# Optimization experiments

Hardware: AMD Instinct MI355X
Metric: run time of the kernel (lower is better)

Reference implementation:

```python
import jax, jax.numpy as jnp
import numpy as np

N = 8192      # atoms
B = 64        # molecules
E = 262144    # edges
S = 4         # species
NMAX = 8      # radial basis size
CUT = 5.0     # cutoff radius
AVG_ATOMS = 128.0
E_SCALE = 1.0
PS_DIM = (S * NMAX) ** 2 * 4  # l_max=3 -> 4 l channels -> 4096
H1, H2 = 1024, 1024
OUT = 1


def _sph_harm(u):
    # real spherical harmonics up to l=3, input unit vectors [E,3] -> [E,16]
    x, y, z = u[:, 0], u[:, 1], u[:, 2]
    x2, y2, z2 = x * x, y * y, z * z
    return jnp.stack([
        0.28209479 * jnp.ones_like(x),
        0.48860251 * y, 0.48860251 * z, 0.48860251 * x,
        1.09254843 * x * y, 1.09254843 * y * z, 0.31539157 * (3.0 * z2 - 1.0),
        1.09254843 * x * z, 0.54627422 * (x2 - y2),
        0.59004359 * y * (3.0 * x2 - y2), 2.89061144 * x * y * z,
        0.45704579 * y * (5.0 * z2 - 1.0), 0.37317633 * z * (5.0 * z2 - 3.0),
        0.45704579 * x * (5.0 * z2 - 1.0), 1.44530572 * z * (x2 - y2),
        0.59004359 * x * (x2 - 3.0 * y2),
    ], axis=-1)


def setup_inputs() -> dict:
    key = jax.random.key(0)
    ks = jax.random.split(key, 12)
    positions = jax.random.normal(ks[0], (N, 3), dtype=jnp.float32) * 1.5  # dense cloud so many pairs < CUT
    cells = jnp.tile(20.0 * jnp.eye(3, dtype=jnp.float32)[None], (B, 1, 1))
    numbers = jax.random.randint(ks[1], (N,), 0, S)
    edge_indices = jax.random.randint(ks[2], (2, E), 0, N)
    edge_offsets = jnp.zeros((E, 3), dtype=jnp.float32)
    batch = jnp.arange(N) // (N // B)
    gamma = 1.0 + 0.1 * jax.random.normal(ks[3], (PS_DIM,), dtype=jnp.float32)
    beta = 0.1 * jax.random.normal(ks[4], (PS_DIM,), dtype=jnp.float32)
    W_ps = jax.random.normal(ks[5], (PS_DIM, OUT), dtype=jnp.float32) / np.sqrt(PS_DIM)
    W1 = jax.random.normal(ks[6], (PS_DIM, H1), dtype=jnp.float32) / np.sqrt(PS_DIM)
    W2 = jax.random.normal(ks[7], (H1, H2), dtype=jnp.float32) / np.sqrt(H1)
    W3 = jax.random.normal(ks[8], (H2, OUT), dtype=jnp.float32) / np.sqrt(H2)
    W_comp = jax.random.normal(ks[9], (S, OUT), dtype=jnp.float32) / np.sqrt(S)
    return dict(positions=positions, cells=cells, numbers=numbers,
                edge_indices=edge_indices, edge_offsets=edge_offsets, batch=batch,
                gamma=gamma, beta=beta, W_ps=W_ps, W1=W1, W2=W2, W3=W3, W_comp=W_comp)


def reference(positions, cells, numbers, edge_indices, edge_offsets, batch,
              gamma, beta, W_ps, W1, W2, W3, W_comp):
    i, j = edge_indices[0], edge_indices[1]  # center, neighbor
    # periodic shift: fractional offsets through the cell of the center's molecule
    shift = jnp.einsum('ec,ecd->ed', edge_offsets, cells[batch[i]])
    rvec = positions[j] - positions[i] + shift                      # [E,3]
    r = jnp.sqrt(jnp.sum(rvec * rvec, axis=-1) + 1e-12)             # [E]
    u = rvec / r[:, None]
    fc = 0.5 * (jnp.cos(jnp.pi * jnp.minimum(r, CUT) / CUT) + 1.0) * (r < CUT)
    n = jnp.arange(1, NMAX + 1, dtype=positions.dtype)
    R = fc[:, None] * jnp.sin(jnp.pi * n[None, :] * r[:, None] / CUT) / r[:, None]  # [E,NMAX]
    Y = _sph_harm(u)                                                # [E,16]
    edge_feat = R[:, :, None] * Y[:, None, :]                       # [E,NMAX,16]
    # spherical expansion c[i, species(j), n, lm] via scatter-add
    seg = i * S + numbers[j]
    c = jax.ops.segment_sum(edge_feat, seg, num_segments=N * S)     # [N*S,NMAX,16]
    c = c.reshape(N, S * NMAX, 16)
    # power spectrum: contract over m within each l block
    bounds = [(0, 1), (1, 4), (4, 9), (9, 16)]
    p = [jnp.einsum('ixm,iym->ixy', c[:, :, s:e], c[:, :, s:e]) for s, e in bounds]
    ps = jnp.stack(p, axis=-1).reshape(N, PS_DIM)                   # [N,4096]
    # LayerNorm (eps=1e-5, affine)
    mu = jnp.mean(ps, axis=-1, keepdims=True)
    var = jnp.var(ps, axis=-1, keepdims=True)
    psn = (ps - mu) / jnp.sqrt(var + 1e-5) * gamma + beta
    # linear branch + MLP branch
    psl = psn @ W_ps                                                # [N,1]
    h = jax.nn.silu(psn @ W1)
    h = jax.nn.silu(h @ W2)
    psnn = h @ W3                                                   # [N,1]
    # pool atomic energies into per-molecule totals (index_add)
    energies = jax.ops.segment_sum(psl + psnn, batch, num_segments=B) / AVG_ATOMS
    # eval path: composition baseline
    comp = jax.ops.segment_sum(jax.nn.one_hot(numbers, S, dtype=psn.dtype), batch, num_segments=B)
    return energies * E_SCALE + comp @ W_comp                       # [B,1]
```

## Files before the change

kernel.cpp:

```cpp
#include <hip/hip_runtime.h>
#include <hip/hip_bf16.h>
#include <math.h>

#define N_ATOMS 8192
#define B_BATCH 64
#define E_EDGES 262144
#define S_SPEC 4
#define NMAX 8
#define PS_DIM 4096
#define PS_K 2304
#define H1_DIM 1024
#define CAP4 48
#define CUTR 5.0f
#define PI_F 3.14159265358979f

typedef __bf16 bf16;
typedef unsigned long long u64;
typedef float floatx4 __attribute__((ext_vector_type(4)));
typedef int intx8 __attribute__((ext_vector_type(8)));
typedef unsigned char u8;

__device__ __forceinline__ void g2lds16(const void* g, void* l) {
    __builtin_amdgcn_global_load_lds(
        (const __attribute__((address_space(1))) void*)g,
        (__attribute__((address_space(3))) void*)l, 16, 0, 0);
}

__device__ __forceinline__ int pk_fp8x4(float a, float b, float c, float d) {
    int lo = __builtin_amdgcn_cvt_pk_fp8_f32(a, b, 0, false);
    return __builtin_amdgcn_cvt_pk_fp8_f32(c, d, lo, true);
}

__global__ __launch_bounds__(256) void prep_kernel(
    const float* __restrict__ pos, const float* __restrict__ cells,
    const int* __restrict__ numbers, const int* __restrict__ ei,
    const float* __restrict__ eo, const int* __restrict__ batch,
    int* __restrict__ cnt, float4* __restrict__ bucket,
    const float* __restrict__ W1, const float* __restrict__ gamma,
    const float* __restrict__ beta, const float* __restrict__ Wps,
    const float* __restrict__ W2,
    u8* __restrict__ Wt1, u8* __restrict__ Wt2, float* __restrict__ b1,
    float* __restrict__ gw, float* __restrict__ S23, float* __restrict__ out)
{
    if (blockIdx.x < 1024) {
        if (blockIdx.x == 0 && threadIdx.x < B_BATCH) out[threadIdx.x] = 0.0f;
        int e = blockIdx.x * 256 + threadIdx.x;
        int i = ei[e];
        int j = ei[E_EDGES + e];
        int b = batch[i];
        const float* cell = cells + b * 9;
        float o0 = eo[e * 3 + 0], o1 = eo[e * 3 + 1], o2 = eo[e * 3 + 2];
        float rv[3];
        #pragma unroll
        for (int d = 0; d < 3; ++d) {
            float shift = o0 * cell[0 * 3 + d] + o1 * cell[1 * 3 + d] + o2 * cell[2 * 3 + d];
            rv[d] = pos[j * 3 + d] - pos[i * 3 + d] + shift;
        }
        float r2 = rv[0] * rv[0] + rv[1] * rv[1] + rv[2] * rv[2] + 1e-12f;
        if (r2 >= CUTR * CUTR) return;
        float r = sqrtf(r2);
        float a1 = r * (PI_F / CUTR);
        int sp = numbers[j];
        int q = i * S_SPEC + sp;
        int slot = atomicAdd(&cnt[q], 1);
        if (slot < CAP4)
            bucket[q * CAP4 + slot] = make_float4(rv[0], rv[1], rv[2], a1);
        return;
    }

    if (blockIdx.x == 4352) {
        __shared__ float rs[8][2];
        int t = threadIdx.x, lane = t & 63, wv = t >> 6;
        float s2 = 0.0f, s3 = 0.0f;
        #pragma unroll
        for (int it = 0; it < 4; ++it) {
            int p4 = it * 256 + t;
            float4 g = *(const float4*)(gamma + p4 * 4);
            float4 bt = *(const float4*)(beta + p4 * 4);
            float4 w = *(const float4*)(Wps + p4 * 4);
            float4 gwv = make_float4(g.x * w.x, g.y * w.y, g.z * w.z, g.w * w.w);
            *(float4*)(gw + p4 * 4) = gwv;
            s2 += gwv.x + gwv.y + gwv.z + gwv.w;
            s3 += bt.x * w.x + bt.y * w.y + bt.z * w.z + bt.w * w.w;
        }
        #pragma unroll
        for (int o = 32; o > 0; o >>= 1) {
            s2 += __shfl_down(s2, o);
            s3 += __shfl_down(s3, o);
        }
        if (lane == 0) { rs[wv][0] = s2; rs[wv][1] = s3; }
        __syncthreads();
        if (t == 0) {
            S23[0] = rs[0][0] + rs[1][0] + rs[2][0] + rs[3][0];
            S23[1] = rs[0][1] + rs[1][1] + rs[2][1] + rs[3][1];
        }
        return;
    }

    __shared__ float tbuf[32][33];
    __shared__ float bred[8][32];
    int wid = blockIdx.x - 1024;
    int by = wid & 31;
    int bx = wid >> 5;
    int tx = threadIdx.x & 31, ty = threadIdx.x >> 5;
    int n0 = by * 32;

    if (bx < 72) {
        int k0 = bx * 32;
        float bacc = 0.0f;
        for (int r = 0; r < 32; r += 8) {
            int kk = ty + r;
            int kp = k0 + kk;
            int u = kp >> 2, lb = kp & 3;
            float val = 0.0f;
            if (u < 528) {
                int x = 0;
                while ((x + 1) * (64 - x) / 2 <= u) ++x;
                int y = x + (u - x * (65 - x) / 2);
                int p1 = x * 128 + y * 4 + lb;
                float w1v = W1[(size_t)p1 * H1_DIM + n0 + tx];
                val = gamma[p1] * w1v;
                bacc += beta[p1] * w1v;
                if (x < y) {
                    int p2 = y * 128 + x * 4 + lb;
                    float w2v = W1[(size_t)p2 * H1_DIM + n0 + tx];
                    val += gamma[p2] * w2v;
                    bacc += beta[p2] * w2v;
                }
            }
            tbuf[kk][tx] = val;
        }
        bred[ty][tx] = bacc;
        __syncthreads();
        if (ty == 0) {
            float s = 0.0f;
            #pragma unroll
            for (int i = 0; i < 8; ++i) s += bred[i][tx];
            atomicAdd(&b1[n0 + tx], s);
        }
        if (threadIdx.x < 64) {
            int nl = threadIdx.x >> 1, cc = threadIdx.x & 1;
            int n = n0 + nl;
            unsigned int w[4];
            #pragma unroll
            for (int g = 0; g < 4; ++g) {
                int kb = cc * 16 + g * 4;
                w[g] = (unsigned int)pk_fp8x4(
                    tbuf[kb + 0][nl] * 64.0f, tbuf[kb + 1][nl] * 64.0f,
                    tbuf[kb + 2][nl] * 64.0f, tbuf[kb + 3][nl] * 64.0f);
            }
            int gc = (k0 >> 4) + cc;
            int gcs = (gc & ~7) | ((gc & 7) ^ (n & 7));
            *(uint4*)(Wt1 + (size_t)n * PS_K + (size_t)gcs * 16) =
                make_uint4(w[0], w[1], w[2], w[3]);
        }
    } else {
        int k0 = (bx - 72) * 32;
        #pragma unroll
        for (int r = 0; r < 32; r += 8)
            tbuf[ty + r][tx] = W2[(size_t)(k0 + ty + r) * H1_DIM + n0 + tx];
        __syncthreads();
        if (threadIdx.x < 64) {
            int nl = threadIdx.x >> 1, cc = threadIdx.x & 1;
            int n = n0 + nl;
            unsigned int w[4];
            #pragma unroll
            for (int g = 0; g < 4; ++g) {
                int kb = cc * 16 + g * 4;
                w[g] = (unsigned int)pk_fp8x4(
                    tbuf[kb + 0][nl] * 32.0f, tbuf[kb + 1][nl] * 32.0f,
                    tbuf[kb + 2][nl] * 32.0f, tbuf[kb + 3][nl] * 32.0f);
            }
            int gc = (k0 >> 4) + cc;
            int gcs = (gc & ~7) | ((gc & 7) ^ (n & 7));
            *(uint4*)(Wt2 + (size_t)n * H1_DIM + (size_t)gcs * 16) =
                make_uint4(w[0], w[1], w[2], w[3]);
        }
    }
}

__global__ __launch_bounds__(256) void accum_ps_kernel(
    const float4* __restrict__ bucket, const int* __restrict__ cnt,
    const float* __restrict__ gw, const float* __restrict__ S23,
    u8* __restrict__ psn, float* __restrict__ psl)
{
    __shared__ __align__(16) float cl[4][32 * 20];
    __shared__ __align__(16) u8 ps_s8[PS_K];
    __shared__ float red[12];

    int t = threadIdx.x;
    int wv = t >> 6, lane = t & 63;
    int atom0 = blockIdx.x * 4;

    {
        int atom = atom0 + wv;
        int sp_l = lane >> 4;
        int nidx = (lane >> 1) & 7;
        float nf = (float)(nidx + 1);
        int par = lane & 1;

        int myCnt = cnt[atom * S_SPEC + sp_l];
        if (myCnt > CAP4) myCnt = CAP4;
        int m1 = max(myCnt, __shfl_xor(myCnt, 16));
        int mx = max(m1, __shfl_xor(m1, 32));

        const float4* q = bucket + (size_t)(atom * S_SPEC + sp_l) * CAP4;
        float acc[8] = {};
        #pragma unroll 2
        for (int e = 0; e < mx; ++e) {
            float4 d = q[e];
            bool valid = e < myCnt;
            float a1 = d.w;
            float inv_r = (PI_F / CUTR) * __frcp_rn(a1);
            float fc = 0.5f * __cosf(a1) + 0.5f;
            float rn = fc * inv_r * __sinf(nf * a1);
            rn = valid ? rn : 0.0f;

            float x = d.x * inv_r, y = d.y * inv_r, z = d.z * inv_r;
            float x2 = x * x, y2 = y * y, z2 = z * z;
            float Ys[8];
            if (par == 0) {
                Ys[0] = 0.28209479f;
                Ys[1] = 0.48860251f * y;
                Ys[2] = 0.48860251f * z;
                Ys[3] = 0.48860251f * x;
                Ys[4] = 1.09254843f * x * y;
                Ys[5] = 1.09254843f * y * z;
                Ys[6] = 0.31539157f * (3.0f * z2 - 1.0f);
                Ys[7] = 1.09254843f * x * z;
            } else {
                Ys[0] = 0.54627422f * (x2 - y2);
                Ys[1] = 0.59004359f * y * (3.0f * x2 - y2);
                Ys[2] = 2.89061144f * x * y * z;
                Ys[3] = 0.45704579f * y * (5.0f * z2 - 1.0f);
                Ys[4] = 0.37317633f * z * (5.0f * z2 - 3.0f);
                Ys[5] = 0.45704579f * x * (5.0f * z2 - 1.0f);
                Ys[6] = 1.44530572f * z * (x2 - y2);
                Ys[7] = 0.59004359f * x * (x2 - 3.0f * y2);
            }
            #pragma unroll
            for (int k = 0; k < 8; ++k) acc[k] += rn * Ys[k];
        }
        int X = sp_l * 8 + nidx;
        float* dst = &cl[wv][X * 20 + par * 8];
        *(float4*)(dst + 0) = make_float4(acc[0], acc[1], acc[2], acc[3]);
        *(float4*)(dst + 4) = make_float4(acc[4], acc[5], acc[6], acc[7]);
    }
    if (t < 48) ((int*)ps_s8)[528 + t] = 0;
    __syncthreads();

    float S2c = S23[0], S3c = S23[1];

    for (int a = 0; a < 4; ++a) {
        int atom = atom0 + a;
        const float* cl_x = cl[a];

        int y = t & 31;
        int xb = t >> 5;
        float4 cya = *(const float4*)&cl_x[y * 20 + 0];
        float4 cyb = *(const float4*)&cl_x[y * 20 + 4];
        float4 cyc = *(const float4*)&cl_x[y * 20 + 8];
        float4 cyd = *(const float4*)&cl_x[y * 20 + 12];

        float ps[4][4];
        float sum = 0.0f, sumsq = 0.0f, S1 = 0.0f;
        #pragma unroll
        for (int q = 0; q < 4; ++q) {
            int x = xb + 8 * q;
            float4 xa = *(const float4*)&cl_x[x * 20 + 0];
            float4 xbv = *(const float4*)&cl_x[x * 20 + 4];
            float4 xc = *(const float4*)&cl_x[x * 20 + 8];
            float4 xd = *(const float4*)&cl_x[x * 20 + 12];
            float s0 = xa.x * cya.x;
            float s1 = xa.y * cya.y + xa.z * cya.z + xa.w * cya.w;
            float s2 = xbv.x * cyb.x + xbv.y * cyb.y + xbv.z * cyb.z + xbv.w * cyb.w
                     + xc.x * cyc.x;
            float s3 = xc.y * cyc.y + xc.z * cyc.z + xc.w * cyc.w
                     + xd.x * cyd.x + xd.y * cyd.y + xd.z * cyd.z + xd.w * cyd.w;
            ps[q][0] = s0; ps[q][1] = s1; ps[q][2] = s2; ps[q][3] = s3;
            sum += s0 + s1 + s2 + s3;
            sumsq += s0 * s0 + s1 * s1 + s2 * s2 + s3 * s3;
            int p = t + 256 * q;
            float4 gwv = *(const float4*)(gw + p * 4);
            S1 += s0 * gwv.x + s1 * gwv.y + s2 * gwv.z + s3 * gwv.w;
        }
        #pragma unroll
        for (int o = 32; o > 0; o >>= 1) {
            sum += __shfl_down(sum, o);
            sumsq += __shfl_down(sumsq, o);
            S1 += __shfl_down(S1, o);
        }
        if ((t & 63) == 0) { red[wv] = sum; red[4 + wv] = sumsq; red[8 + wv] = S1; }
        __syncthreads();
        float tot = red[0] + red[1] + red[2] + red[3];
        float totsq = red[4] + red[5] + red[6] + red[7];
        float S1t = red[8] + red[9] + red[10] + red[11];
        float mu = tot * (1.0f / PS_DIM);
        float var = totsq * (1.0f / PS_DIM) - mu * mu;
        float inv = rsqrtf(var + 1e-5f);
        if (t == 0) psl[atom] = inv * (S1t - mu * S2c) + S3c;

        #pragma unroll
        for (int q = 0; q < 4; ++q) {
            int p = t + 256 * q;
            float z0 = (ps[q][0] - mu) * inv;
            float z1 = (ps[q][1] - mu) * inv;
            float z2 = (ps[q][2] - mu) * inv;
            float z3 = (ps[q][3] - mu) * inv;
            int x = p >> 5, yy = p & 31;
            if (x <= yy) {
                int u = x * (65 - x) / 2 + (yy - x);
                ((int*)ps_s8)[u] = pk_fp8x4(z0, z1, z2, z3);
            }
        }
        __syncthreads();
        u8* rowp = psn + (size_t)atom * PS_K;
        if (t < PS_K / 16) {
            int gcs = (t & ~7) | ((t & 7) ^ (atom & 7));
            *(uint4*)(rowp + (size_t)gcs * 16) = *(const uint4*)(ps_s8 + (size_t)t * 16);
        }
    }
}

__global__ __launch_bounds__(256) void gemm_f8_kernel(
    const u8* __restrict__ A, const u8* __restrict__ Bt,
    u8* __restrict__ H, const float* __restrict__ b1,
    int M, int Nc, int K, float invs)
{
    __shared__ __align__(16) char smem[65536];
    int tid = threadIdx.x;
    int bm = blockIdx.x, bn = blockIdx.y;
    int wave = tid >> 6, lane = tid & 63;
    int wm = (wave >> 1) * 64, wn = (wave & 1) * 64;
    int lm = lane & 15, quad = lane >> 4;

    floatx4 acc[4][4] = {};
    const int rowA0 = bm * 128, rowB0 = bn * 128;
    const size_t stride = (size_t)K;
    const char* Ab = (const char*)A + (size_t)rowA0 * stride;
    const char* Bb = (const char*)Bt + (size_t)rowB0 * stride;
    const int sA = 0x7F7F7F7F, sB = 0x7F7F7F7F;

    for (int k0 = 0; k0 < K; k0 += 256) {
        #pragma unroll
        for (int s = 0; s < 8; ++s) {
            int L = s * 256 + tid;
            int row = L >> 4, boff = (L & 15) * 16;
            int lbase = (s * 256 + wave * 64) * 16;
            g2lds16(Ab + (size_t)row * stride + k0 + boff, smem + lbase);
        }
        #pragma unroll
        for (int s = 0; s < 8; ++s) {
            int L = s * 256 + tid;
            int row = L >> 4, boff = (L & 15) * 16;
            int lbase = (s * 256 + wave * 64) * 16;
            g2lds16(Bb + (size_t)row * stride + k0 + boff, smem + 32768 + lbase);
        }
        __syncthreads();
        int key = lm & 7;
        int c0 = (2 * quad) ^ key, c1 = (2 * quad + 1) ^ key;
        #pragma unroll
        for (int h = 0; h < 2; ++h) {
            intx8 af[4], bfr[4];
            #pragma unroll
            for (int mi = 0; mi < 4; ++mi) {
                const char* base = smem + (wm + mi * 16 + lm) * 256 + h * 128;
                uint4 lo = *(const uint4*)(base + c0 * 16);
                uint4 hi = *(const uint4*)(base + c1 * 16);
                af[mi][0] = lo.x; af[mi][1] = lo.y; af[mi][2] = lo.z; af[mi][3] = lo.w;
                af[mi][4] = hi.x; af[mi][5] = hi.y; af[mi][6] = hi.z; af[mi][7] = hi.w;
            }
            #pragma unroll
            for (int ni = 0; ni < 4; ++ni) {
                const char* base = smem + 32768 + (wn + ni * 16 + lm) * 256 + h * 128;
                uint4 lo = *(const uint4*)(base + c0 * 16);
                uint4 hi = *(const uint4*)(base + c1 * 16);
                bfr[ni][0] = lo.x; bfr[ni][1] = lo.y; bfr[ni][2] = lo.z; bfr[ni][3] = lo.w;
                bfr[ni][4] = hi.x; bfr[ni][5] = hi.y; bfr[ni][6] = hi.z; bfr[ni][7] = hi.w;
            }
            #pragma unroll
            for (int mi = 0; mi < 4; ++mi)
                #pragma unroll
                for (int ni = 0; ni < 4; ++ni)
                    acc[mi][ni] = __builtin_amdgcn_mfma_scale_f32_16x16x128_f8f6f4(
                        af[mi], bfr[ni], acc[mi][ni], 0, 0, 0, sA, 0, sB);
        }
        __syncthreads();
    }

    u8* Cs8 = (u8*)smem;
    #pragma unroll
    for (int mi = 0; mi < 4; ++mi)
        #pragma unroll
        for (int ni = 0; ni < 4; ++ni) {
            float bv = b1[bn * 128 + wn + ni * 16 + lm];
            #pragma unroll
            for (int r = 0; r < 4; ++r) {
                int row = wm + mi * 16 + quad * 4 + r;
                int col = wn + ni * 16 + lm;
                float v = acc[mi][ni][r] * invs + bv;
                v = v / (1.0f + __expf(-v));
                int pk = __builtin_amdgcn_cvt_pk_fp8_f32(v, 0.0f, 0, false);
                Cs8[row * 128 + col] = (u8)(pk & 0xFF);
            }
        }
    __syncthreads();
    #pragma unroll
    for (int c2 = 0; c2 < 4; ++c2) {
        int L = c2 * 256 + tid;
        int row = L >> 3, cc = L & 7;
        int gcs = cc ^ (row & 7);
        *(uint4*)(H + (size_t)(rowA0 + row) * Nc + (size_t)(bn * 8 + gcs) * 16) =
            *(const uint4*)(Cs8 + (size_t)L * 16);
    }
}

__global__ __launch_bounds__(256) void gemm2_fused_kernel(
    const u8* __restrict__ A, const u8* __restrict__ Bt,
    const float* __restrict__ W3, const float* __restrict__ psl,
    const int* __restrict__ numbers, const float* __restrict__ Wcomp,
    float* __restrict__ out, int Nc, int K, float invs)
{
    __shared__ __align__(16) char smem[65536];
    int tid = threadIdx.x;
    int bm = blockIdx.x, bn = blockIdx.y;
    int wave = tid >> 6, lane = tid & 63;
    int wm = (wave >> 1) * 64, wn = (wave & 1) * 64;
    int lm = lane & 15, quad = lane >> 4;

    floatx4 acc[4][4] = {};
    const int rowA0 = bm * 128, rowB0 = bn * 128;
    const size_t stride = (size_t)K;
    const char* Ab = (const char*)A + (size_t)rowA0 * stride;
    const char* Bb = (const char*)Bt + (size_t)rowB0 * stride;
    const int sA = 0x7F7F7F7F, sB = 0x7F7F7F7F;

    for (int k0 = 0; k0 < K; k0 += 256) {
        #pragma unroll
        for (int s = 0; s < 8; ++s) {
            int L = s * 256 + tid;
            int row = L >> 4, boff = (L & 15) * 16;
            int lbase = (s * 256 + wave * 64) * 16;
            g2lds16(Ab + (size_t)row * stride + k0 + boff, smem + lbase);
        }
        #pragma unroll
        for (int s = 0; s < 8; ++s) {
            int L = s * 256 + tid;
            int row = L >> 4, boff = (L & 15) * 16;
            int lbase = (s * 256 + wave * 64) * 16;
            g2lds16(Bb + (size_t)row * stride + k0 + boff, smem + 32768 + lbase);
        }
        __syncthreads();
        int key = lm & 7;
        int c0 = (2 * quad) ^ key, c1 = (2 * quad + 1) ^ key;
        #pragma unroll
        for (int h = 0; h < 2; ++h) {
            intx8 af[4], bfr[4];
            #pragma unroll
            for (int mi = 0; mi < 4; ++mi) {
                const char* base = smem + (wm + mi * 16 + lm) * 256 + h * 128;
                uint4 lo = *(const uint4*)(base + c0 * 16);
                uint4 hi = *(const uint4*)(base + c1 * 16);
                af[mi][0] = lo.x; af[mi][1] = lo.y; af[mi][2] = lo.z; af[mi][3] = lo.w;
                af[mi][4] = hi.x; af[mi][5] = hi.y; af[mi][6] = hi.z; af[mi][7] = hi.w;
            }
            #pragma unroll
            for (int ni = 0; ni < 4; ++ni) {
                const char* base = smem + 32768 + (wn + ni * 16 + lm) * 256 + h * 128;
                uint4 lo = *(const uint4*)(base + c0 * 16);
                uint4 hi = *(const uint4*)(base + c1 * 16);
                bfr[ni][0] = lo.x; bfr[ni][1] = lo.y; bfr[ni][2] = lo.z; bfr[ni][3] = lo.w;
                bfr[ni][4] = hi.x; bfr[ni][5] = hi.y; bfr[ni][6] = hi.z; bfr[ni][7] = hi.w;
            }
            #pragma unroll
            for (int mi = 0; mi < 4; ++mi)
                #pragma unroll
                for (int ni = 0; ni < 4; ++ni)
                    acc[mi][ni] = __builtin_amdgcn_mfma_scale_f32_16x16x128_f8f6f4(
                        af[mi], bfr[ni], acc[mi][ni], 0, 0, 0, sA, 0, sB);
        }
        __syncthreads();
    }

    float lt = 0.0f;
    #pragma unroll
    for (int ni = 0; ni < 4; ++ni) {
        float w3v = W3[bn * 128 + wn + ni * 16 + lm];
        #pragma unroll
        for (int mi = 0; mi < 4; ++mi)
            #pragma unroll
            for (int r = 0; r < 4; ++r) {
                float v = acc[mi][ni][r] * invs;
                v = v / (1.0f + __expf(-v));
                lt += v * w3v;
            }
    }
    #pragma unroll
    for (int o = 32; o > 0; o >>= 1) lt += __shfl_down(lt, o);
    float* wsum = (float*)smem;
    int* c4 = ((int*)smem) + 8;
    float* shp = ((float*)smem) + 12;
    if (tid < S_SPEC) c4[tid] = 0;
    if (lane == 0) wsum[wave] = lt;
    __syncthreads();
    if (tid == 0)
        atomicAdd(&out[bm],
                  (wsum[0] + wsum[1] + wsum[2] + wsum[3]) * (1.0f / 128.0f));
    if (bn == 0) {
        if (tid < 128) {
            int a = bm * 128 + tid;
            float e = psl[a];
            atomicAdd(&c4[numbers[a]], 1);
            #pragma unroll
            for (int o = 32; o > 0; o >>= 1) e += __shfl_down(e, o);
            if ((tid & 63) == 0) shp[tid >> 6] = e;
        }
        __syncthreads();
        if (tid == 0) {
            float r = (shp[0] + shp[1]) * (1.0f / 128.0f);
            #pragma unroll
            for (int s = 0; s < S_SPEC; ++s) r += (float)c4[s] * Wcomp[s];
            atomicAdd(&out[bm], r);
        }
    }
}

extern "C" void kernel_launch(void* const* d_in, const int* in_sizes, int n_in,
                              void* d_out, int out_size, void* d_ws, size_t ws_size,
                              hipStream_t stream)
{
    const float* positions = (const float*)d_in[0];
    const float* cells     = (const float*)d_in[1];
    const int*   numbers   = (const int*)d_in[2];
    const int*   ei        = (const int*)d_in[3];
    const float* eo        = (const float*)d_in[4];
    const int*   batch     = (const int*)d_in[5];
    const float* gamma     = (const float*)d_in[6];
    const float* beta      = (const float*)d_in[7];
    const float* W_ps      = (const float*)d_in[8];
    const float* W1        = (const float*)d_in[9];
    const float* W2        = (const float*)d_in[10];
    const float* W3        = (const float*)d_in[11];
    const float* W_comp    = (const float*)d_in[12];
    float* out = (float*)d_out;

    char* ws = (char*)d_ws;
    float4* bucket = (float4*)ws;  ws += (size_t)N_ATOMS * S_SPEC * CAP4 * 16;
    u8*    psn  = (u8*)ws;     ws += (size_t)N_ATOMS * PS_K;
    u8*    h1   = (u8*)ws;     ws += (size_t)N_ATOMS * H1_DIM;
    u8*    Wt1  = (u8*)ws;     ws += (size_t)H1_DIM * PS_K;
    u8*    Wt2  = (u8*)ws;     ws += (size_t)H1_DIM * H1_DIM;
    float* psl  = (float*)ws;  ws += (size_t)N_ATOMS * 4;
    int*   cnt  = (int*)ws;    ws += (size_t)N_ATOMS * S_SPEC * 4;
    float* b1   = (float*)ws;  ws += (size_t)H1_DIM * 4;
    float* gw   = (float*)ws;  ws += (size_t)PS_DIM * 4;
    float* S23  = (float*)ws;  ws += 2 * 4;

    hipMemsetAsync(cnt, 0, (N_ATOMS * S_SPEC + H1_DIM) * sizeof(int), stream);

    prep_kernel<<<4353, 256, 0, stream>>>(
        positions, cells, numbers, ei, eo, batch, cnt, bucket,
        W1, gamma, beta, W_ps, W2, Wt1, Wt2, b1, gw, S23, out);

    accum_ps_kernel<<<N_ATOMS / 4, 256, 0, stream>>>(
        bucket, cnt, gw, S23, psn, psl);

    gemm_f8_kernel<<<dim3(N_ATOMS / 128, H1_DIM / 128), 256, 0, stream>>>(
        psn, Wt1, h1, b1, N_ATOMS, H1_DIM, PS_K, 1.0f / 64.0f);

    gemm2_fused_kernel<<<dim3(N_ATOMS / 128, H1_DIM / 128), 256, 0, stream>>>(
        h1, Wt2, W3, psl, numbers, W_comp, out, H1_DIM, H1_DIM, 1.0f / 32.0f);
}
```

Measured before the change: 183.9 us.

## Fuse all stages into one persistent cooperative kernel with grid syncs

```diff
diff --git a/kernel.cpp b/kernel.cpp
--- a/kernel.cpp
+++ b/kernel.cpp
@@ -1,6 +1,9 @@
 #include <hip/hip_runtime.h>
 #include <hip/hip_bf16.h>
+#include <hip/hip_cooperative_groups.h>
 #include <math.h>
+
+namespace cg = cooperative_groups;
 
 #define N_ATOMS 8192
 #define B_BATCH 64
@@ -14,8 +17,6 @@
 #define CUTR 5.0f
 #define PI_F 3.14159265358979f
 
-typedef __bf16 bf16;
-typedef unsigned long long u64;
 typedef float floatx4 __attribute__((ext_vector_type(4)));
 typedef int intx8 __attribute__((ext_vector_type(8)));
 typedef unsigned char u8;
@@ -31,7 +32,7 @@
     return __builtin_amdgcn_cvt_pk_fp8_f32(c, d, lo, true);
 }
 
-__global__ __launch_bounds__(256) void prep_kernel(
+__global__ __launch_bounds__(256, 2) void fused_all(
     const float* __restrict__ pos, const float* __restrict__ cells,
     const int* __restrict__ numbers, const int* __restrict__ ei,
     const float* __restrict__ eo, const int* __restrict__ batch,
@@ -40,488 +41,506 @@
     const float* __restrict__ beta, const float* __restrict__ Wps,
     const float* __restrict__ W2,
     u8* __restrict__ Wt1, u8* __restrict__ Wt2, float* __restrict__ b1,
-    float* __restrict__ gw, float* __restrict__ S23, float* __restrict__ out)
-{
-    if (blockIdx.x < 1024) {
-        if (blockIdx.x == 0 && threadIdx.x < B_BATCH) out[threadIdx.x] = 0.0f;
-        int e = blockIdx.x * 256 + threadIdx.x;
-        int i = ei[e];
-        int j = ei[E_EDGES + e];
-        int b = batch[i];
-        const float* cell = cells + b * 9;
-        float o0 = eo[e * 3 + 0], o1 = eo[e * 3 + 1], o2 = eo[e * 3 + 2];
-        float rv[3];
-        #pragma unroll
-        for (int d = 0; d < 3; ++d) {
-            float shift = o0 * cell[0 * 3 + d] + o1 * cell[1 * 3 + d] + o2 * cell[2 * 3 + d];
-            rv[d] = pos[j * 3 + d] - pos[i * 3 + d] + shift;
-        }
-        float r2 = rv[0] * rv[0] + rv[1] * rv[1] + rv[2] * rv[2] + 1e-12f;
-        if (r2 >= CUTR * CUTR) return;
-        float r = sqrtf(r2);
-        float a1 = r * (PI_F / CUTR);
-        int sp = numbers[j];
-        int q = i * S_SPEC + sp;
-        int slot = atomicAdd(&cnt[q], 1);
-        if (slot < CAP4)
-            bucket[q * CAP4 + slot] = make_float4(rv[0], rv[1], rv[2], a1);
-        return;
-    }
-
-    if (blockIdx.x == 4352) {
-        __shared__ float rs[8][2];
-        int t = threadIdx.x, lane = t & 63, wv = t >> 6;
-        float s2 = 0.0f, s3 = 0.0f;
-        #pragma unroll
-        for (int it = 0; it < 4; ++it) {
-            int p4 = it * 256 + t;
-            float4 g = *(const float4*)(gamma + p4 * 4);
-            float4 bt = *(const float4*)(beta + p4 * 4);
-            float4 w = *(const float4*)(Wps + p4 * 4);
-            float4 gwv = make_float4(g.x * w.x, g.y * w.y, g.z * w.z, g.w * w.w);
-            *(float4*)(gw + p4 * 4) = gwv;
-            s2 += gwv.x + gwv.y + gwv.z + gwv.w;
-            s3 += bt.x * w.x + bt.y * w.y + bt.z * w.z + bt.w * w.w;
-        }
-        #pragma unroll
-        for (int o = 32; o > 0; o >>= 1) {
-            s2 += __shfl_down(s2, o);
-            s3 += __shfl_down(s3, o);
-        }
-        if (lane == 0) { rs[wv][0] = s2; rs[wv][1] = s3; }
-        __syncthreads();
-        if (t == 0) {
-            S23[0] = rs[0][0] + rs[1][0] + rs[2][0] + rs[3][0];
-            S23[1] = rs[0][1] + rs[1][1] + rs[2][1] + rs[3][1];
-        }
-        return;
-    }
-
-    __shared__ float tbuf[32][33];
-    __shared__ float bred[8][32];
-    int wid = blockIdx.x - 1024;
-    int by = wid & 31;
-    int bx = wid >> 5;
-    int tx = threadIdx.x & 31, ty = threadIdx.x >> 5;
-    int n0 = by * 32;
-
-    if (bx < 72) {
-        int k0 = bx * 32;
-        float bacc = 0.0f;
-        for (int r = 0; r < 32; r += 8) {
-            int kk = ty + r;
-            int kp = k0 + kk;
-            int u = kp >> 2, lb = kp & 3;
-            float val = 0.0f;
-            if (u < 528) {
-                int x = 0;
-                while ((x + 1) * (64 - x) / 2 <= u) ++x;
-                int y = x + (u - x * (65 - x) / 2);
-                int p1 = x * 128 + y * 4 + lb;
-                float w1v = W1[(size_t)p1 * H1_DIM + n0 + tx];
-                val = gamma[p1] * w1v;
-                bacc += beta[p1] * w1v;
-                if (x < y) {
-                    int p2 = y * 128 + x * 4 + lb;
-                    float w2v = W1[(size_t)p2 * H1_DIM + n0 + tx];
-                    val += gamma[p2] * w2v;
-                    bacc += beta[p2] * w2v;
-                }
-            }
-            tbuf[kk][tx] = val;
-        }
-        bred[ty][tx] = bacc;
-        __syncthreads();
-        if (ty == 0) {
-            float s = 0.0f;
-            #pragma unroll
-            for (int i = 0; i < 8; ++i) s += bred[i][tx];
-            atomicAdd(&b1[n0 + tx], s);
-        }
-        if (threadIdx.x < 64) {
-            int nl = threadIdx.x >> 1, cc = threadIdx.x & 1;
-            int n = n0 + nl;
-            unsigned int w[4];
-            #pragma unroll
-            for (int g = 0; g < 4; ++g) {
-                int kb = cc * 16 + g * 4;
-                w[g] = (unsigned int)pk_fp8x4(
-                    tbuf[kb + 0][nl] * 64.0f, tbuf[kb + 1][nl] * 64.0f,
-                    tbuf[kb + 2][nl] * 64.0f, tbuf[kb + 3][nl] * 64.0f);
-            }
-            int gc = (k0 >> 4) + cc;
-            int gcs = (gc & ~7) | ((gc & 7) ^ (n & 7));
-            *(uint4*)(Wt1 + (size_t)n * PS_K + (size_t)gcs * 16) =
-                make_uint4(w[0], w[1], w[2], w[3]);
-        }
-    } else {
-        int k0 = (bx - 72) * 32;
-        #pragma unroll
-        for (int r = 0; r < 32; r += 8)
-            tbuf[ty + r][tx] = W2[(size_t)(k0 + ty + r) * H1_DIM + n0 + tx];
-        __syncthreads();
-        if (threadIdx.x < 64) {
-            int nl = threadIdx.x >> 1, cc = threadIdx.x & 1;
-            int n = n0 + nl;
-            unsigned int w[4];
-            #pragma unroll
-            for (int g = 0; g < 4; ++g) {
-                int kb = cc * 16 + g * 4;
-                w[g] = (unsigned int)pk_fp8x4(
-                    tbuf[kb + 0][nl] * 32.0f, tbuf[kb + 1][nl] * 32.0f,
-                    tbuf[kb + 2][nl] * 32.0f, tbuf[kb + 3][nl] * 32.0f);
-            }
-            int gc = (k0 >> 4) + cc;
-            int gcs = (gc & ~7) | ((gc & 7) ^ (n & 7));
-            *(uint4*)(Wt2 + (size_t)n * H1_DIM + (size_t)gcs * 16) =
-                make_uint4(w[0], w[1], w[2], w[3]);
-        }
-    }
-}
-
-__global__ __launch_bounds__(256) void accum_ps_kernel(
-    const float4* __restrict__ bucket, const int* __restrict__ cnt,
-    const float* __restrict__ gw, const float* __restrict__ S23,
-    u8* __restrict__ psn, float* __restrict__ psl)
-{
-    __shared__ __align__(16) float cl[4][32 * 20];
-    __shared__ __align__(16) u8 ps_s8[PS_K];
-    __shared__ float red[12];
-
-    int t = threadIdx.x;
-    int wv = t >> 6, lane = t & 63;
-    int atom0 = blockIdx.x * 4;
-
-    {
-        int atom = atom0 + wv;
-        int sp_l = lane >> 4;
-        int nidx = (lane >> 1) & 7;
-        float nf = (float)(nidx + 1);
-        int par = lane & 1;
-
-        int myCnt = cnt[atom * S_SPEC + sp_l];
-        if (myCnt > CAP4) myCnt = CAP4;
-        int m1 = max(myCnt, __shfl_xor(myCnt, 16));
-        int mx = max(m1, __shfl_xor(m1, 32));
-
-        const float4* q = bucket + (size_t)(atom * S_SPEC + sp_l) * CAP4;
-        float acc[8] = {};
-        #pragma unroll 2
-        for (int e = 0; e < mx; ++e) {
-            float4 d = q[e];
-            bool valid = e < myCnt;
-            float a1 = d.w;
-            float inv_r = (PI_F / CUTR) * __frcp_rn(a1);
-            float fc = 0.5f * __cosf(a1) + 0.5f;
-            float rn = fc * inv_r * __sinf(nf * a1);
-            rn = valid ? rn : 0.0f;
-
-            float x = d.x * inv_r, y = d.y * inv_r, z = d.z * inv_r;
-            float x2 = x * x, y2 = y * y, z2 = z * z;
-            float Ys[8];
-            if (par == 0) {
-                Ys[0] = 0.28209479f;
-                Ys[1] = 0.48860251f * y;
-                Ys[2] = 0.48860251f * z;
-                Ys[3] = 0.48860251f * x;
-                Ys[4] = 1.09254843f * x * y;
-                Ys[5] = 1.09254843f * y * z;
-                Ys[6] = 0.31539157f * (3.0f * z2 - 1.0f);
-                Ys[7] = 1.09254843f * x * z;
-            } else {
-                Ys[0] = 0.54627422f * (x2 - y2);
-                Ys[1] = 0.59004359f * y * (3.0f * x2 - y2);
-                Ys[2] = 2.89061144f * x * y * z;
-                Ys[3] = 0.45704579f * y * (5.0f * z2 - 1.0f);
-                Ys[4] = 0.37317633f * z * (5.0f * z2 - 3.0f);
-                Ys[5] = 0.45704579f * x * (5.0f * z2 - 1.0f);
-                Ys[6] = 1.44530572f * z * (x2 - y2);
-                Ys[7] = 0.59004359f * x * (x2 - 3.0f * y2);
-            }
-            #pragma unroll
-            for (int k = 0; k < 8; ++k) acc[k] += rn * Ys[k];
-        }
-        int X = sp_l * 8 + nidx;
-        float* dst = &cl[wv][X * 20 + par * 8];
-        *(float4*)(dst + 0) = make_float4(acc[0], acc[1], acc[2], acc[3]);
-        *(float4*)(dst + 4) = make_float4(acc[4], acc[5], acc[6], acc[7]);
-    }
-    if (t < 48) ((int*)ps_s8)[528 + t] = 0;
-    __syncthreads();
-
-    float S2c = S23[0], S3c = S23[1];
-
-    for (int a = 0; a < 4; ++a) {
-        int atom = atom0 + a;
-        const float* cl_x = cl[a];
-
-        int y = t & 31;
-        int xb = t >> 5;
-        float4 cya = *(const float4*)&cl_x[y * 20 + 0];
-        float4 cyb = *(const float4*)&cl_x[y * 20 + 4];
-        float4 cyc = *(const float4*)&cl_x[y * 20 + 8];
-        float4 cyd = *(const float4*)&cl_x[y * 20 + 12];
-
-        float ps[4][4];
-        float sum = 0.0f, sumsq = 0.0f, S1 = 0.0f;
-        #pragma unroll
-        for (int q = 0; q < 4; ++q) {
-            int x = xb + 8 * q;
-            float4 xa = *(const float4*)&cl_x[x * 20 + 0];
-            float4 xbv = *(const float4*)&cl_x[x * 20 + 4];
-            float4 xc = *(const float4*)&cl_x[x * 20 + 8];
-            float4 xd = *(const float4*)&cl_x[x * 20 + 12];
-            float s0 = xa.x * cya.x;
-            float s1 = xa.y * cya.y + xa.z * cya.z + xa.w * cya.w;
-            float s2 = xbv.x * cyb.x + xbv.y * cyb.y + xbv.z * cyb.z + xbv.w * cyb.w
-                     + xc.x * cyc.x;
-            float s3 = xc.y * cyc.y + xc.z * cyc.z + xc.w * cyc.w
-                     + xd.x * cyd.x + xd.y * cyd.y + xd.z * cyd.z + xd.w * cyd.w;
-            ps[q][0] = s0; ps[q][1] = s1; ps[q][2] = s2; ps[q][3] = s3;
-            sum += s0 + s1 + s2 + s3;
-            sumsq += s0 * s0 + s1 * s1 + s2 * s2 + s3 * s3;
-            int p = t + 256 * q;
-            float4 gwv = *(const float4*)(gw + p * 4);
-            S1 += s0 * gwv.x + s1 * gwv.y + s2 * gwv.z + s3 * gwv.w;
-        }
-        #pragma unroll
-        for (int o = 32; o > 0; o >>= 1) {
-            sum += __shfl_down(sum, o);
-            sumsq += __shfl_down(sumsq, o);
-            S1 += __shfl_down(S1, o);
-        }
-        if ((t & 63) == 0) { red[wv] = sum; red[4 + wv] = sumsq; red[8 + wv] = S1; }
-        __syncthreads();
-        float tot = red[0] + red[1] + red[2] + red[3];
-        float totsq = red[4] + red[5] + red[6] + red[7];
-        float S1t = red[8] + red[9] + red[10] + red[11];
-        float mu = tot * (1.0f / PS_DIM);
-        float var = totsq * (1.0f / PS_DIM) - mu * mu;
-        float inv = rsqrtf(var + 1e-5f);
-        if (t == 0) psl[atom] = inv * (S1t - mu * S2c) + S3c;
-
-        #pragma unroll
-        for (int q = 0; q < 4; ++q) {
-            int p = t + 256 * q;
-            float z0 = (ps[q][0] - mu) * inv;
-            float z1 = (ps[q][1] - mu) * inv;
-            float z2 = (ps[q][2] - mu) * inv;
-            float z3 = (ps[q][3] - mu) * inv;
-            int x = p >> 5, yy = p & 31;
-            if (x <= yy) {
-                int u = x * (65 - x) / 2 + (yy - x);
-                ((int*)ps_s8)[u] = pk_fp8x4(z0, z1, z2, z3);
-            }
-        }
-        __syncthreads();
-        u8* rowp = psn + (size_t)atom * PS_K;
-        if (t < PS_K / 16) {
-            int gcs = (t & ~7) | ((t & 7) ^ (atom & 7));
-            *(uint4*)(rowp + (size_t)gcs * 16) = *(const uint4*)(ps_s8 + (size_t)t * 16);
-        }
-    }
-}
-
-__global__ __launch_bounds__(256) void gemm_f8_kernel(
-    const u8* __restrict__ A, const u8* __restrict__ Bt,
-    u8* __restrict__ H, const float* __restrict__ b1,
-    int M, int Nc, int K, float invs)
+    float* __restrict__ gw, float* __restrict__ S23,
+    u8* __restrict__ psn, float* __restrict__ psl, u8* __restrict__ h1,
+    const float* __restrict__ W3, const float* __restrict__ Wcomp,
+    float* __restrict__ out)
 {
     __shared__ __align__(16) char smem[65536];
-    int tid = threadIdx.x;
-    int bm = blockIdx.x, bn = blockIdx.y;
-    int wave = tid >> 6, lane = tid & 63;
-    int wm = (wave >> 1) * 64, wn = (wave & 1) * 64;
-    int lm = lane & 15, quad = lane >> 4;
-
-    floatx4 acc[4][4] = {};
-    const int rowA0 = bm * 128, rowB0 = bn * 128;
-    const size_t stride = (size_t)K;
-    const char* Ab = (const char*)A + (size_t)rowA0 * stride;
-    const char* Bb = (const char*)Bt + (size_t)rowB0 * stride;
-    const int sA = 0x7F7F7F7F, sB = 0x7F7F7F7F;
-
-    for (int k0 = 0; k0 < K; k0 += 256) {
+    cg::grid_group grid = cg::this_grid();
+    const int nblk = gridDim.x;
+    const int tid = threadIdx.x;
+
+    {
+        int total = N_ATOMS * S_SPEC + H1_DIM;
+        for (int idx = blockIdx.x * 256 + tid; idx < total; idx += nblk * 256)
+            cnt[idx] = 0;
+        if (blockIdx.x == 0 && tid < B_BATCH) out[tid] = 0.0f;
+    }
+    __threadfence();
+    grid.sync();
+
+    {
+        float (*tbuf)[33] = (float(*)[33])smem;
+        float (*bred)[32] = (float(*)[32])(smem + 4224);
+        float (*rs)[2]    = (float(*)[2])(smem + 5248);
+
+        for (int vb = blockIdx.x; vb < 4353; vb += nblk) {
+            if (vb < 1024) {
+                int e = vb * 256 + tid;
+                int i = ei[e];
+                int j = ei[E_EDGES + e];
+                int b = batch[i];
+                const float* cell = cells + b * 9;
+                float o0 = eo[e * 3 + 0], o1 = eo[e * 3 + 1], o2 = eo[e * 3 + 2];
+                float rv[3];
+                #pragma unroll
+                for (int d = 0; d < 3; ++d) {
+                    float shift = o0 * cell[0 * 3 + d] + o1 * cell[1 * 3 + d]
+                                + o2 * cell[2 * 3 + d];
+                    rv[d] = pos[j * 3 + d] - pos[i * 3 + d] + shift;
+                }
+                float r2 = rv[0] * rv[0] + rv[1] * rv[1] + rv[2] * rv[2] + 1e-12f;
+                if (r2 < CUTR * CUTR) {
+                    float r = sqrtf(r2);
+                    float a1 = r * (PI_F / CUTR);
+                    int sp = numbers[j];
+                    int q = i * S_SPEC + sp;
+                    int slot = atomicAdd(&cnt[q], 1);
+                    if (slot < CAP4)
+                        bucket[q * CAP4 + slot] = make_float4(rv[0], rv[1], rv[2], a1);
+                }
+                continue;
+            }
+            if (vb == 4352) {
+                int lane = tid & 63, wv = tid >> 6;
+                float s2 = 0.0f, s3 = 0.0f;
+                #pragma unroll
+                for (int it = 0; it < 4; ++it) {
+                    int p4 = it * 256 + tid;
+                    float4 g = *(const float4*)(gamma + p4 * 4);
+                    float4 bt = *(const float4*)(beta + p4 * 4);
+                    float4 w = *(const float4*)(Wps + p4 * 4);
+                    float4 gwv = make_float4(g.x * w.x, g.y * w.y, g.z * w.z, g.w * w.w);
+                    *(float4*)(gw + p4 * 4) = gwv;
+                    s2 += gwv.x + gwv.y + gwv.z + gwv.w;
+                    s3 += bt.x * w.x + bt.y * w.y + bt.z * w.z + bt.w * w.w;
+                }
+                #pragma unroll
+                for (int o = 32; o > 0; o >>= 1) {
+                    s2 += __shfl_down(s2, o);
+                    s3 += __shfl_down(s3, o);
+                }
+                if (lane == 0) { rs[wv][0] = s2; rs[wv][1] = s3; }
+                __syncthreads();
+                if (tid == 0) {
+                    S23[0] = rs[0][0] + rs[1][0] + rs[2][0] + rs[3][0];
+                    S23[1] = rs[0][1] + rs[1][1] + rs[2][1] + rs[3][1];
+                }
+                __syncthreads();
+                continue;
+            }
+            int wid = vb - 1024;
+            int by = wid & 31;
+            int bx = wid >> 5;
+            int tx = tid & 31, ty = tid >> 5;
+            int n0 = by * 32;
+
+            if (bx < 72) {
+                int k0 = bx * 32;
+                float bacc = 0.0f;
+                for (int r = 0; r < 32; r += 8) {
+                    int kk = ty + r;
+                    int kp = k0 + kk;
+                    int u = kp >> 2, lb = kp & 3;
+                    float val = 0.0f;
+                    if (u < 528) {
+                        int x = 0;
+                        while ((x + 1) * (64 - x) / 2 <= u) ++x;
+                        int y = x + (u - x * (65 - x) / 2);
+                        int p1 = x * 128 + y * 4 + lb;
+                        float w1v = W1[(size_t)p1 * H1_DIM + n0 + tx];
+                        val = gamma[p1] * w1v;
+                        bacc += beta[p1] * w1v;
+                        if (x < y) {
+                            int p2 = y * 128 + x * 4 + lb;
+                            float w2v = W1[(size_t)p2 * H1_DIM + n0 + tx];
+                            val += gamma[p2] * w2v;
+                            bacc += beta[p2] * w2v;
+                        }
+                    }
+                    tbuf[kk][tx] = val;
+                }
+                bred[ty][tx] = bacc;
+                __syncthreads();
+                if (ty == 0) {
+                    float s = 0.0f;
+                    #pragma unroll
+                    for (int i = 0; i < 8; ++i) s += bred[i][tx];
+                    atomicAdd(&b1[n0 + tx], s);
+                }
+                if (tid < 64) {
+                    int nl = tid >> 1, cc = tid & 1;
+                    int n = n0 + nl;
+                    unsigned int w[4];
+                    #pragma unroll
+                    for (int g = 0; g < 4; ++g) {
+                        int kb = cc * 16 + g * 4;
+                        w[g] = (unsigned int)pk_fp8x4(
+                            tbuf[kb + 0][nl] * 64.0f, tbuf[kb + 1][nl] * 64.0f,
+                            tbuf[kb + 2][nl] * 64.0f, tbuf[kb + 3][nl] * 64.0f);
+                    }
+                    int gc = (k0 >> 4) + cc;
+                    int gcs = (gc & ~7) | ((gc & 7) ^ (n & 7));
+                    *(uint4*)(Wt1 + (size_t)n * PS_K + (size_t)gcs * 16) =
+                        make_uint4(w[0], w[1], w[2], w[3]);
+                }
+                __syncthreads();
+            } else {
+                int k0 = (bx - 72) * 32;
+                #pragma unroll
+                for (int r = 0; r < 32; r += 8)
+                    tbuf[ty + r][tx] = W2[(size_t)(k0 + ty + r) * H1_DIM + n0 + tx];
+                __syncthreads();
+                if (tid < 64) {
+                    int nl = tid >> 1, cc = tid & 1;
+                    int n = n0 + nl;
+                    unsigned int w[4];
+                    #pragma unroll
+                    for (int g = 0; g < 4; ++g) {
+                        int kb = cc * 16 + g * 4;
+                        w[g] = (unsigned int)pk_fp8x4(
+                            tbuf[kb + 0][nl] * 32.0f, tbuf[kb + 1][nl] * 32.0f,
+                            tbuf[kb + 2][nl] * 32.0f, tbuf[kb + 3][nl] * 32.0f);
+                    }
+                    int gc = (k0 >> 4) + cc;
+                    int gcs = (gc & ~7) | ((gc & 7) ^ (n & 7));
+                    *(uint4*)(Wt2 + (size_t)n * H1_DIM + (size_t)gcs * 16) =
+                        make_uint4(w[0], w[1], w[2], w[3]);
+                }
+                __syncthreads();
+            }
+        }
+    }
+    __threadfence();
+    grid.sync();
+
+    {
+        float (*cl)[640] = (float(*)[640])smem;
+        u8* ps_s8 = (u8*)(smem + 10240);
+        float* red = (float*)(smem + 12544);
+
+        int wv = tid >> 6, lane = tid & 63;
+        float S2c = S23[0], S3c = S23[1];
+
+        for (int vb = blockIdx.x; vb < N_ATOMS / 4; vb += nblk) {
+            int atom0 = vb * 4;
+            {
+                int atom = atom0 + wv;
+                int sp_l = lane >> 4;
+                int nidx = (lane >> 1) & 7;
+                float nf = (float)(nidx + 1);
+                int par = lane & 1;
+
+                int myCnt = cnt[atom * S_SPEC + sp_l];
+                if (myCnt > CAP4) myCnt = CAP4;
+                int m1 = max(myCnt, __shfl_xor(myCnt, 16));
+                int mx = max(m1, __shfl_xor(m1, 32));
+
+                const float4* q = bucket + (size_t)(atom * S_SPEC + sp_l) * CAP4;
+                float acc[8] = {};
+                #pragma unroll 2
+                for (int e = 0; e < mx; ++e) {
+                    float4 d = q[e];
+                    bool valid = e < myCnt;
+                    float a1 = d.w;
+                    float inv_r = (PI_F / CUTR) * __frcp_rn(a1);
+                    float fc = 0.5f * __cosf(a1) + 0.5f;
+                    float rn = fc * inv_r * __sinf(nf * a1);
+                    rn = valid ? rn : 0.0f;
+
+                    float x = d.x * inv_r, y = d.y * inv_r, z = d.z * inv_r;
+                    float x2 = x * x, y2 = y * y, z2 = z * z;
+                    float Ys[8];
+                    if (par == 0) {
+                        Ys[0] = 0.28209479f;
+                        Ys[1] = 0.48860251f * y;
+                        Ys[2] = 0.48860251f * z;
+                        Ys[3] = 0.48860251f * x;
+                        Ys[4] = 1.09254843f * x * y;
+                        Ys[5] = 1.09254843f * y * z;
+                        Ys[6] = 0.31539157f * (3.0f * z2 - 1.0f);
+                        Ys[7] = 1.09254843f * x * z;
+                    } else {
+                        Ys[0] = 0.54627422f * (x2 - y2);
+                        Ys[1] = 0.59004359f * y * (3.0f * x2 - y2);
+                        Ys[2] = 2.89061144f * x * y * z;
+                        Ys[3] = 0.45704579f * y * (5.0f * z2 - 1.0f);
+                        Ys[4] = 0.37317633f * z * (5.0f * z2 - 3.0f);
+                        Ys[5] = 0.45704579f * x * (5.0f * z2 - 1.0f);
+                        Ys[6] = 1.44530572f * z * (x2 - y2);
+                        Ys[7] = 0.59004359f * x * (x2 - 3.0f * y2);
+                    }
+                    #pragma unroll
+                    for (int k = 0; k < 8; ++k) acc[k] += rn * Ys[k];
+                }
+                int X = sp_l * 8 + nidx;
+                float* dst = &cl[wv][X * 20 + par * 8];
+                *(float4*)(dst + 0) = make_float4(acc[0], acc[1], acc[2], acc[3]);
+                *(float4*)(dst + 4) = make_float4(acc[4], acc[5], acc[6], acc[7]);
+            }
+            if (tid < 48) ((int*)ps_s8)[528 + tid] = 0;
+            __syncthreads();
+
+            for (int a = 0; a < 4; ++a) {
+                int atom = atom0 + a;
+                const float* cl_x = cl[a];
+
+                int y = tid & 31;
+                int xb = tid >> 5;
+                float4 cya = *(const float4*)&cl_x[y * 20 + 0];
+                float4 cyb = *(const float4*)&cl_x[y * 20 + 4];
+                float4 cyc = *(const float4*)&cl_x[y * 20 + 8];
+                float4 cyd = *(const float4*)&cl_x[y * 20 + 12];
+
+                float ps[4][4];
+                float sum = 0.0f, sumsq = 0.0f, S1 = 0.0f;
+                #pragma unroll
+                for (int q = 0; q < 4; ++q) {
+                    int x = xb + 8 * q;
+                    float4 xa = *(const float4*)&cl_x[x * 20 + 0];
+                    float4 xbv = *(const float4*)&cl_x[x * 20 + 4];
+                    float4 xc = *(const float4*)&cl_x[x * 20 + 8];
+                    float4 xd = *(const float4*)&cl_x[x * 20 + 12];
+                    float s0 = xa.x * cya.x;
+                    float s1 = xa.y * cya.y + xa.z * cya.z + xa.w * cya.w;
+                    float s2 = xbv.x * cyb.x + xbv.y * cyb.y + xbv.z * cyb.z
+                             + xbv.w * cyb.w + xc.x * cyc.x;
+                    float s3 = xc.y * cyc.y + xc.z * cyc.z + xc.w * cyc.w
+                             + xd.x * cyd.x + xd.y * cyd.y + xd.z * cyd.z + xd.w * cyd.w;
+                    ps[q][0] = s0; ps[q][1] = s1; ps[q][2] = s2; ps[q][3] = s3;
+                    sum += s0 + s1 + s2 + s3;
+                    sumsq += s0 * s0 + s1 * s1 + s2 * s2 + s3 * s3;
+                    int p = tid + 256 * q;
+                    float4 gwv = *(const float4*)(gw + p * 4);
+                    S1 += s0 * gwv.x + s1 * gwv.y + s2 * gwv.z + s3 * gwv.w;
+                }
+                #pragma unroll
+                for (int o = 32; o > 0; o >>= 1) {
+                    sum += __shfl_down(sum, o);
+                    sumsq += __shfl_down(sumsq, o);
+                    S1 += __shfl_down(S1, o);
+                }
+                if ((tid & 63) == 0) { red[wv] = sum; red[4 + wv] = sumsq; red[8 + wv] = S1; }
+                __syncthreads();
+                float tot = red[0] + red[1] + red[2] + red[3];
+                float totsq = red[4] + red[5] + red[6] + red[7];
+                float S1t = red[8] + red[9] + red[10] + red[11];
+                float mu = tot * (1.0f / PS_DIM);
+                float var = totsq * (1.0f / PS_DIM) - mu * mu;
+                float inv = rsqrtf(var + 1e-5f);
+                if (tid == 0) psl[atom] = inv * (S1t - mu * S2c) + S3c;
+
+                #pragma unroll
+                for (int q = 0; q < 4; ++q) {
+                    int p = tid + 256 * q;
+                    float z0 = (ps[q][0] - mu) * inv;
+                    float z1 = (ps[q][1] - mu) * inv;
+                    float z2 = (ps[q][2] - mu) * inv;
+                    float z3 = (ps[q][3] - mu) * inv;
+                    int x = p >> 5, yy = p & 31;
+                    if (x <= yy) {
+                        int u = x * (65 - x) / 2 + (yy - x);
+                        ((int*)ps_s8)[u] = pk_fp8x4(z0, z1, z2, z3);
+                    }
+                }
+                __syncthreads();
+                u8* rowp = psn + (size_t)atom * PS_K;
+                if (tid < PS_K / 16) {
+                    int gcs = (tid & ~7) | ((tid & 7) ^ (atom & 7));
+                    *(uint4*)(rowp + (size_t)gcs * 16) =
+                        *(const uint4*)(ps_s8 + (size_t)tid * 16);
+                }
+            }
+            __syncthreads();
+        }
+    }
+    __threadfence();
+    grid.sync();
+
+    for (int vb = blockIdx.x; vb < 512; vb += nblk) {
+        int bm = vb & 63, bn = vb >> 6;
+        int wave = tid >> 6, lane = tid & 63;
+        int wm = (wave >> 1) * 64, wn = (wave & 1) * 64;
+        int lm = lane & 15, quad = lane >> 4;
+
+        floatx4 acc[4][4] = {};
+        const int rowA0 = bm * 128, rowB0 = bn * 128;
+        const size_t stride = (size_t)PS_K;
+        const char* Ab = (const char*)psn + (size_t)rowA0 * stride;
+        const char* Bb = (const char*)Wt1 + (size_t)rowB0 * stride;
+        const int sA = 0x7F7F7F7F, sB = 0x7F7F7F7F;
+
+        __syncthreads();
+        for (int k0 = 0; k0 < PS_K; k0 += 256) {
+            #pragma unroll
+            for (int s = 0; s < 8; ++s) {
+                int L = s * 256 + tid;
+                int row = L >> 4, boff = (L & 15) * 16;
+                int lbase = (s * 256 + wave * 64) * 16;
+                g2lds16(Ab + (size_t)row * stride + k0 + boff, smem + lbase);
+            }
+            #pragma unroll
+            for (int s = 0; s < 8; ++s) {
+                int L = s * 256 + tid;
+                int row = L >> 4, boff = (L & 15) * 16;
+                int lbase = (s * 256 + wave * 64) * 16;
+                g2lds16(Bb + (size_t)row * stride + k0 + boff, smem + 32768 + lbase);
+            }
+            __syncthreads();
+            int key = lm & 7;
+            int c0 = (2 * quad) ^ key, c1 = (2 * quad + 1) ^ key;
+            #pragma unroll
+            for (int h = 0; h < 2; ++h) {
+                intx8 af[4], bfr[4];
+                #pragma unroll
+                for (int mi = 0; mi < 4; ++mi) {
+                    const char* base = smem + (wm + mi * 16 + lm) * 256 + h * 128;
+                    uint4 lo = *(const uint4*)(base + c0 * 16);
+                    uint4 hi = *(const uint4*)(base + c1 * 16);
+                    af[mi][0] = lo.x; af[mi][1] = lo.y; af[mi][2] = lo.z; af[mi][3] = lo.w;
+                    af[mi][4] = hi.x; af[mi][5] = hi.y; af[mi][6] = hi.z; af[mi][7] = hi.w;
+                }
+                #pragma unroll
+                for (int ni = 0; ni < 4; ++ni) {
+                    const char* base = smem + 32768 + (wn + ni * 16 + lm) * 256 + h * 128;
+                    uint4 lo = *(const uint4*)(base + c0 * 16);
+                    uint4 hi = *(const uint4*)(base + c1 * 16);
+                    bfr[ni][0] = lo.x; bfr[ni][1] = lo.y; bfr[ni][2] = lo.z; bfr[ni][3] = lo.w;
+                    bfr[ni][4] = hi.x; bfr[ni][5] = hi.y; bfr[ni][6] = hi.z; bfr[ni][7] = hi.w;
+                }
+                #pragma unroll
+                for (int mi = 0; mi < 4; ++mi)
+                    #pragma unroll
+                    for (int ni = 0; ni < 4; ++ni)
+                        acc[mi][ni] = __builtin_amdgcn_mfma_scale_f32_16x16x128_f8f6f4(
+                            af[mi], bfr[ni], acc[mi][ni], 0, 0, 0, sA, 0, sB);
+            }
+            __syncthreads();
+        }
+
+        u8* Cs8 = (u8*)smem;
         #pragma unroll
-        for (int s = 0; s < 8; ++s) {
-            int L = s * 256 + tid;
-            int row = L >> 4, boff = (L & 15) * 16;
-            int lbase = (s * 256 + wave * 64) * 16;
-            g2lds16(Ab + (size_t)row * stride + k0 + boff, smem + lbase);
-        }
+        for (int mi = 0; mi < 4; ++mi)
+            #pragma unroll
+            for (int ni = 0; ni < 4; ++ni) {
+                float bv = b1[bn * 128 + wn + ni * 16 + lm];
+                #pragma unroll
+                for (int r = 0; r < 4; ++r) {
+                    int row = wm + mi * 16 + quad * 4 + r;
+                    int col = wn + ni * 16 + lm;
+                    float v = acc[mi][ni][r] * (1.0f / 64.0f) + bv;
+                    v = v / (1.0f + __expf(-v));
+                    int pk = __builtin_amdgcn_cvt_pk_fp8_f32(v, 0.0f, 0, false);
+                    Cs8[row * 128 + col] = (u8)(pk & 0xFF);
+                }
+            }
+        __syncthreads();
         #pragma unroll
-        for (int s = 0; s < 8; ++s) {
-            int L = s * 256 + tid;
-            int row = L >> 4, boff = (L & 15) * 16;
-            int lbase = (s * 256 + wave * 64) * 16;
-            g2lds16(Bb + (size_t)row * stride + k0 + boff, smem + 32768 + lbase);
-        }
+        for (int c2 = 0; c2 < 4; ++c2) {
+            int L = c2 * 256 + tid;
+            int row = L >> 3, cc = L & 7;
+            int gcs = cc ^ (row & 7);
+            *(uint4*)(h1 + (size_t)(rowA0 + row) * H1_DIM + (size_t)(bn * 8 + gcs) * 16) =
+                *(const uint4*)(Cs8 + (size_t)L * 16);
+        }
+    }
+    __threadfence();
+    grid.sync();
+
+    for (int vb = blockIdx.x; vb < 512; vb += nblk) {
+        int bm = vb & 63, bn = vb >> 6;
+        int wave = tid >> 6, lane = tid & 63;
+        int wm = (wave >> 1) * 64, wn = (wave & 1) * 64;
+        int lm = lane & 15, quad = lane >> 4;
+
+        floatx4 acc[4][4] = {};
+        const int rowA0 = bm * 128, rowB0 = bn * 128;
+        const size_t stride = (size_t)H1_DIM;
+        const char* Ab = (const char*)h1 + (size_t)rowA0 * stride;
+        const char* Bb = (const char*)Wt2 + (size_t)rowB0 * stride;
+        const int sA = 0x7F7F7F7F, sB = 0x7F7F7F7F;
+
         __syncthreads();
-        int key = lm & 7;
-        int c0 = (2 * quad) ^ key, c1 = (2 * quad + 1) ^ key;
-        #pragma unroll
-        for (int h = 0; h < 2; ++h) {
-            intx8 af[4], bfr[4];
-            #pragma unroll
-            for (int mi = 0; mi < 4; ++mi) {
-                const char* base = smem + (wm + mi * 16 + lm) * 256 + h * 128;
-                uint4 lo = *(const uint4*)(base + c0 * 16);
-                uint4 hi = *(const uint4*)(base + c1 * 16);
-                af[mi][0] = lo.x; af[mi][1] = lo.y; af[mi][2] = lo.z; af[mi][3] = lo.w;
-                af[mi][4] = hi.x; af[mi][5] = hi.y; af[mi][6] = hi.z; af[mi][7] = hi.w;
-            }
-            #pragma unroll
-            for (int ni = 0; ni < 4; ++ni) {
-                const char* base = smem + 32768 + (wn + ni * 16 + lm) * 256 + h * 128;
-                uint4 lo = *(const uint4*)(base + c0 * 16);
-                uint4 hi = *(const uint4*)(base + c1 * 16);
-                bfr[ni][0] = lo.x; bfr[ni][1] = lo.y; bfr[ni][2] = lo.z; bfr[ni][3] = lo.w;
-                bfr[ni][4] = hi.x; bfr[ni][5] = hi.y; bfr[ni][6] = hi.z; bfr[ni][7] = hi.w;
-            }
-            #pragma unroll
-            for (int mi = 0; mi < 4; ++mi)
-                #pragma unroll
-                for (int ni = 0; ni < 4; ++ni)
-                    acc[mi][ni] = __builtin_amdgcn_mfma_scale_f32_16x16x128_f8f6f4(
-                        af[mi], bfr[ni], acc[mi][ni], 0, 0, 0, sA, 0, sB);
-        }
-        __syncthreads();
-    }
-
-    u8* Cs8 = (u8*)smem;
-    #pragma unroll
-    for (int mi = 0; mi < 4; ++mi)
+        for (int k0 = 0; k0 < H1_DIM; k0 += 256) {
+            #pragma unroll
+            for (int s = 0; s < 8; ++s) {
+                int L = s * 256 + tid;
+                int row = L >> 4, boff = (L & 15) * 16;
+                int lbase = (s * 256 + wave * 64) * 16;
+                g2lds16(Ab + (size_t)row * stride + k0 + boff, smem + lbase);
+            }
+            #pragma unroll
+            for (int s = 0; s < 8; ++s) {
+                int L = s * 256 + tid;
+                int row = L >> 4, boff = (L & 15) * 16;
+                int lbase = (s * 256 + wave * 64) * 16;
+                g2lds16(Bb + (size_t)row * stride + k0 + boff, smem + 32768 + lbase);
+            }
+            __syncthreads();
+            int key = lm & 7;
+            int c0 = (2 * quad) ^ key, c1 = (2 * quad + 1) ^ key;
+            #pragma unroll
+            for (int h = 0; h < 2; ++h) {
+                intx8 af[4], bfr[4];
+                #pragma unroll
+                for (int mi = 0; mi < 4; ++mi) {
+                    const char* base = smem + (wm + mi * 16 + lm) * 256 + h * 128;
+                    uint4 lo = *(const uint4*)(base + c0 * 16);
+                    uint4 hi = *(const uint4*)(base + c1 * 16);
+                    af[mi][0] = lo.x; af[mi][1] = lo.y; af[mi][2] = lo.z; af[mi][3] = lo.w;
+                    af[mi][4] = hi.x; af[mi][5] = hi.y; af[mi][6] = hi.z; af[mi][7] = hi.w;
+                }
+                #pragma unroll
+                for (int ni = 0; ni < 4; ++ni) {
+                    const char* base = smem + 32768 + (wn + ni * 16 + lm) * 256 + h * 128;
+                    uint4 lo = *(const uint4*)(base + c0 * 16);
+                    uint4 hi = *(const uint4*)(base + c1 * 16);
+                    bfr[ni][0] = lo.x; bfr[ni][1] = lo.y; bfr[ni][2] = lo.z; bfr[ni][3] = lo.w;
+                    bfr[ni][4] = hi.x; bfr[ni][5] = hi.y; bfr[ni][6] = hi.z; bfr[ni][7] = hi.w;
+                }
+                #pragma unroll
+                for (int mi = 0; mi < 4; ++mi)
+                    #pragma unroll
+                    for (int ni = 0; ni < 4; ++ni)
+                        acc[mi][ni] = __builtin_amdgcn_mfma_scale_f32_16x16x128_f8f6f4(
+                            af[mi], bfr[ni], acc[mi][ni], 0, 0, 0, sA, 0, sB);
+            }
+            __syncthreads();
+        }
+
+        float lt = 0.0f;
         #pragma unroll
         for (int ni = 0; ni < 4; ++ni) {
-            float bv = b1[bn * 128 + wn + ni * 16 + lm];
-            #pragma unroll
-            for (int r = 0; r < 4; ++r) {
-                int row = wm + mi * 16 + quad * 4 + r;
-                int col = wn + ni * 16 + lm;
-                float v = acc[mi][ni][r] * invs + bv;
-                v = v / (1.0f + __expf(-v));
-                int pk = __builtin_amdgcn_cvt_pk_fp8_f32(v, 0.0f, 0, false);
-                Cs8[row * 128 + col] = (u8)(pk & 0xFF);
-            }
-        }
-    __syncthreads();
-    #pragma unroll
-    for (int c2 = 0; c2 < 4; ++c2) {
-        int L = c2 * 256 + tid;
-        int row = L >> 3, cc = L & 7;
-        int gcs = cc ^ (row & 7);
-        *(uint4*)(H + (size_t)(rowA0 + row) * Nc + (size_t)(bn * 8 + gcs) * 16) =
-            *(const uint4*)(Cs8 + (size_t)L * 16);
-    }
-}
-
-__global__ __launch_bounds__(256) void gemm2_fused_kernel(
-    const u8* __restrict__ A, const u8* __restrict__ Bt,
-    const float* __restrict__ W3, const float* __restrict__ psl,
-    const int* __restrict__ numbers, const float* __restrict__ Wcomp,
-    float* __restrict__ out, int Nc, int K, float invs)
-{
-    __shared__ __align__(16) char smem[65536];
-    int tid = threadIdx.x;
-    int bm = blockIdx.x, bn = blockIdx.y;
-    int wave = tid >> 6, lane = tid & 63;
-    int wm = (wave >> 1) * 64, wn = (wave & 1) * 64;
-    int lm = lane & 15, quad = lane >> 4;
-
-    floatx4 acc[4][4] = {};
-    const int rowA0 = bm * 128, rowB0 = bn * 128;
-    const size_t stride = (size_t)K;
-    const char* Ab = (const char*)A + (size_t)rowA0 * stride;
-    const char* Bb = (const char*)Bt + (size_t)rowB0 * stride;
-    const int sA = 0x7F7F7F7F, sB = 0x7F7F7F7F;
-
-    for (int k0 = 0; k0 < K; k0 += 256) {
+            float w3v = W3[bn * 128 + wn + ni * 16 + lm];
+            #pragma unroll
+            for (int mi = 0; mi < 4; ++mi)
+                #pragma unroll
+                for (int r = 0; r < 4; ++r) {
+                    float v = acc[mi][ni][r] * (1.0f / 32.0f);
+                    v = v / (1.0f + __expf(-v));
+                    lt += v * w3v;
+                }
+        }
         #pragma unroll
-        for (int s = 0; s < 8; ++s) {
-            int L = s * 256 + tid;
-            int row = L >> 4, boff = (L & 15) * 16;
-            int lbase = (s * 256 + wave * 64) * 16;
-            g2lds16(Ab + (size_t)row * stride + k0 + boff, smem + lbase);
-        }
-        #pragma unroll
-        for (int s = 0; s < 8; ++s) {
-            int L = s * 256 + tid;
-            int row = L >> 4, boff = (L & 15) * 16;
-            int lbase = (s * 256 + wave * 64) * 16;
-            g2lds16(Bb + (size_t)row * stride + k0 + boff, smem + 32768 + lbase);
-        }
+        for (int o = 32; o > 0; o >>= 1) lt += __shfl_down(lt, o);
+        float* wsum = (float*)smem;
+        int* c4 = ((int*)smem) + 8;
+        float* shp = ((float*)smem) + 12;
+        if (tid < S_SPEC) c4[tid] = 0;
+        if (lane == 0) wsum[wave] = lt;
         __syncthreads();
-        int key = lm & 7;
-        int c0 = (2 * quad) ^ key, c1 = (2 * quad + 1) ^ key;
-        #pragma unroll
-        for (int h = 0; h < 2; ++h) {
-            intx8 af[4], bfr[4];
-            #pragma unroll
-            for (int mi = 0; mi < 4; ++mi) {
-                const char* base = smem + (wm + mi * 16 + lm) * 256 + h * 128;
-                uint4 lo = *(const uint4*)(base + c0 * 16);
-                uint4 hi = *(const uint4*)(base + c1 * 16);
-                af[mi][0] = lo.x; af[mi][1] = lo.y; af[mi][2] = lo.z; af[mi][3] = lo.w;
-                af[mi][4] = hi.x; af[mi][5] = hi.y; af[mi][6] = hi.z; af[mi][7] = hi.w;
-            }
-            #pragma unroll
-            for (int ni = 0; ni < 4; ++ni) {
-                const char* base = smem + 32768 + (wn + ni * 16 + lm) * 256 + h * 128;
-                uint4 lo = *(const uint4*)(base + c0 * 16);
-                uint4 hi = *(const uint4*)(base + c1 * 16);
-                bfr[ni][0] = lo.x; bfr[ni][1] = lo.y; bfr[ni][2] = lo.z; bfr[ni][3] = lo.w;
-                bfr[ni][4] = hi.x; bfr[ni][5] = hi.y; bfr[ni][6] = hi.z; bfr[ni][7] = hi.w;
-            }
-            #pragma unroll
-            for (int mi = 0; mi < 4; ++mi)
-                #pragma unroll
-                for (int ni = 0; ni < 4; ++ni)
-                    acc[mi][ni] = __builtin_amdgcn_mfma_scale_f32_16x16x128_f8f6f4(
-                        af[mi], bfr[ni], acc[mi][ni], 0, 0, 0, sA, 0, sB);
+        if (tid == 0)
+            atomicAdd(&out[bm],
+                      (wsum[0] + wsum[1] + wsum[2] + wsum[3]) * (1.0f / 128.0f));
+        if (bn == 0) {
+            if (tid < 128) {
+                int a = bm * 128 + tid;
+                float e = psl[a];
+                atomicAdd(&c4[numbers[a]], 1);
+                #pragma unroll
+                for (int o = 32; o > 0; o >>= 1) e += __shfl_down(e, o);
+                if ((tid & 63) == 0) shp[tid >> 6] = e;
+            }
+            __syncthreads();
+            if (tid == 0) {
+                float r = (shp[0] + shp[1]) * (1.0f / 128.0f);
+                #pragma unroll
+                for (int s = 0; s < S_SPEC; ++s) r += (float)c4[s] * Wcomp[s];
+                atomicAdd(&out[bm], r);
+            }
         }
         __syncthreads();
-    }
-
-    float lt = 0.0f;
-    #pragma unroll
-    for (int ni = 0; ni < 4; ++ni) {
-        float w3v = W3[bn * 128 + wn + ni * 16 + lm];
-        #pragma unroll
-        for (int mi = 0; mi < 4; ++mi)
-            #pragma unroll
-            for (int r = 0; r < 4; ++r) {
-                float v = acc[mi][ni][r] * invs;
-                v = v / (1.0f + __expf(-v));
-                lt += v * w3v;
-            }
-    }
-    #pragma unroll
-    for (int o = 32; o > 0; o >>= 1) lt += __shfl_down(lt, o);
-    float* wsum = (float*)smem;
-    int* c4 = ((int*)smem) + 8;
-    float* shp = ((float*)smem) + 12;
-    if (tid < S_SPEC) c4[tid] = 0;
-    if (lane == 0) wsum[wave] = lt;
-    __syncthreads();
-    if (tid == 0)
-        atomicAdd(&out[bm],
-                  (wsum[0] + wsum[1] + wsum[2] + wsum[3]) * (1.0f / 128.0f));
-    if (bn == 0) {
-        if (tid < 128) {
-            int a = bm * 128 + tid;
-            float e = psl[a];
-            atomicAdd(&c4[numbers[a]], 1);
-            #pragma unroll
-            for (int o = 32; o > 0; o >>= 1) e += __shfl_down(e, o);
-            if ((tid & 63) == 0) shp[tid >> 6] = e;
-        }
-        __syncthreads();
-        if (tid == 0) {
-            float r = (shp[0] + shp[1]) * (1.0f / 128.0f);
-            #pragma unroll
-            for (int s = 0; s < S_SPEC; ++s) r += (float)c4[s] * Wcomp[s];
-            atomicAdd(&out[bm], r);
-        }
     }
 }
 
@@ -556,18 +575,26 @@
     float* gw   = (float*)ws;  ws += (size_t)PS_DIM * 4;
     float* S23  = (float*)ws;  ws += 2 * 4;
 
-    hipMemsetAsync(cnt, 0, (N_ATOMS * S_SPEC + H1_DIM) * sizeof(int), stream);
-
-    prep_kernel<<<4353, 256, 0, stream>>>(
-        positions, cells, numbers, ei, eo, batch, cnt, bucket,
-        W1, gamma, beta, W_ps, W2, Wt1, Wt2, b1, gw, S23, out);
-
-    accum_ps_kernel<<<N_ATOMS / 4, 256, 0, stream>>>(
-        bucket, cnt, gw, S23, psn, psl);
-
-    gemm_f8_kernel<<<dim3(N_ATOMS / 128, H1_DIM / 128), 256, 0, stream>>>(
-        psn, Wt1, h1, b1, N_ATOMS, H1_DIM, PS_K, 1.0f / 64.0f);
-
-    gemm2_fused_kernel<<<dim3(N_ATOMS / 128, H1_DIM / 128), 256, 0, stream>>>(
-        h1, Wt2, W3, psl, numbers, W_comp, out, H1_DIM, H1_DIM, 1.0f / 32.0f);
+    static int nblk = 0;
+    if (nblk == 0) {
+        int perCU = 0;
+        if (hipOccupancyMaxActiveBlocksPerMultiprocessor(&perCU, fused_all, 256, 0)
+                == hipSuccess && perCU >= 1) {
+            nblk = perCU * 256;
+            if (nblk > 512) nblk = 512;
+        } else {
+            nblk = 256;
+        }
+    }
+
+    void* args[] = {
+        (void*)&positions, (void*)&cells, (void*)&numbers, (void*)&ei,
+        (void*)&eo, (void*)&batch, (void*)&cnt, (void*)&bucket,
+        (void*)&W1, (void*)&gamma, (void*)&beta, (void*)&W_ps, (void*)&W2,
+        (void*)&Wt1, (void*)&Wt2, (void*)&b1, (void*)&gw, (void*)&S23,
+        (void*)&psn, (void*)&psl, (void*)&h1,
+        (void*)&W3, (void*)&W_comp, (void*)&out
+    };
+    hipLaunchCooperativeKernel((const void*)fused_all, dim3(nblk), dim3(256),
+                               args, 0, stream);
 }
```

After: 485.1 us. +163.8%, slower.
